# Kernel optimization log

Hardware: AMD Instinct MI355X
Metric: run time of the kernel (lower is better)

Reference implementation:

```python
import jax, jax.numpy as jnp
import numpy as np

EPS = 0.1  # residual scale from __init__


def setup_inputs() -> dict:
    key = jax.random.key(0)
    ks = jax.random.split(key, 13)
    T, B, E = 8, 4096, 16          # terms, batch(queries), predicates(edges)
    F = 1024                        # feature_dim = 2*emb_dim (emb_dim=512)
    M = 2 * F + 2                   # message_dim = 4*emb_dim + 2 = 2050
    H = 4096                        # hidden_dim

    def lin(k, fan_in, shape):
        return jax.random.normal(k, shape, jnp.float32) / np.sqrt(fan_in)

    return {
        "term_emb": jax.random.normal(ks[0], (T, B, F), jnp.float32),
        "pred_emb": jax.random.normal(ks[1], (E, B, F), jnp.float32),
        "W1": lin(ks[2], M, (M, H)),
        "b1": jnp.zeros((H,), jnp.float32),
        "W2": lin(ks[3], H, (H, F)),
        "b2": jnp.zeros((F,), jnp.float32),
        "M1": lin(ks[4], F, (F, H)),
        "mb1": jnp.zeros((H,), jnp.float32),
        "M2": lin(ks[5], H, (H, F)),
        "mb2": jnp.zeros((F,), jnp.float32),
        "head_idx": jax.random.randint(ks[6], (E,), 0, T, jnp.int32),
        "tail_idx": jax.random.randint(ks[7], (E,), 0, T, jnp.int32),
        "sign_bits": jax.random.randint(ks[8], (E,), 0, 2, jnp.int32),
    }


def reference(term_emb, pred_emb, W1, b1, W2, b2, M1, mb1, M2, mb2,
              head_idx, tail_idx, sign_bits):
    # term_emb: [T,B,F], pred_emb: [E,B,F]
    T = term_emb.shape[0]
    E, B, F = pred_emb.shape
    dt = pred_emb.dtype

    sign = (1.0 - 2.0 * sign_bits.astype(dt))[:, None, None]   # [E,1,1], +-1
    ones = jnp.ones((E, B, 1), dt)
    s_ones = sign * ones                                        # [E,B,1]

    h = term_emb[head_idx]                                      # gather [E,B,F]
    t = term_emb[tail_idx]                                      # gather [E,B,F]

    # message to head: [head_emb, pred_emb, +1, sign]
    # message to tail: [tail_emb, pred_emb, -1, sign]
    msg_h = jnp.concatenate([h, pred_emb, ones, s_ones], axis=-1)   # [E,B,M]
    msg_t = jnp.concatenate([t, pred_emb, -ones, s_ones], axis=-1)  # [E,B,M]

    msgs = jnp.concatenate([msg_h, msg_t], axis=0)              # [2E,B,M]
    seg = jnp.concatenate([head_idx, tail_idx], axis=0)         # [2E]
    agg = jax.ops.segment_sum(msgs, seg, num_segments=T)        # [T,B,M]

    # encoder MLP + eps residual
    enc = jax.nn.relu(agg @ W1 + b1) @ W2 + b2                  # [T,B,F]
    x = enc + EPS * term_emb

    # update MLP (layers == 1)
    out = jax.nn.relu(x @ M1 + mb1) @ M2 + mb2                  # [T,B,F]
    return out
```

## Files before the change

### kernel.cpp

```cpp
#include <hip/hip_runtime.h>
#include <hip/hip_bf16.h>
#include <cstdint>

typedef unsigned short u16;
typedef __attribute__((ext_vector_type(8))) u16 u16x8;
typedef __attribute__((ext_vector_type(8))) short s16x8;
typedef __attribute__((ext_vector_type(4))) float f32x4;

#define AS1(p) ((const __attribute__((address_space(1))) void*)(p))
#define AS3(p) ((__attribute__((address_space(3))) void*)(p))

__device__ __forceinline__ u16 f2bf(float f){
  union{float f; uint32_t i;} x; x.f = f;
  uint32_t r = x.i + 0x7fff + ((x.i>>16)&1);
  return (u16)(r>>16);
}

__global__ void transpose_f32_bf16(const float* __restrict__ in, u16* __restrict__ out,
                                   int K, int N){
  __shared__ u16 tile[32][33];
  const int tid = threadIdx.x;
  const int bx = blockIdx.x, by = blockIdx.y;
  const int xl = tid & 31, yl = tid >> 5;
  #pragma unroll
  for (int r = 0; r < 4; ++r){
    int y = by*32 + yl + r*8;
    tile[yl + r*8][xl] = f2bf(in[(size_t)y*N + bx*32 + xl]);
  }
  __syncthreads();
  #pragma unroll
  for (int r = 0; r < 4; ++r){
    int oy = bx*32 + yl + r*8;
    int ox = by*32 + xl;
    out[(size_t)oy*K + ox] = tile[xl][yl + r*8];
  }
}

__global__ void build_bias1(const float* __restrict__ W1, const float* __restrict__ b1,
                            const int* __restrict__ head, const int* __restrict__ tail,
                            const int* __restrict__ sign, float* __restrict__ bias1){
  int idx = blockIdx.x*256 + threadIdx.x;
  int t = idx >> 12, h = idx & 4095;
  float cH = 0.f, cS = 0.f;
  #pragma unroll
  for (int e = 0; e < 16; ++e){
    float s = 1.f - 2.f*(float)sign[e];
    if (head[e] == t){ cH += 1.f; cS += s; }
    if (tail[e] == t){ cH -= 1.f; cS += s; }
  }
  bias1[idx] = b1[h] + cH*W1[(size_t)2048*4096 + h] + cS*W1[(size_t)2049*4096 + h];
}

__global__ void build_x1(const float* __restrict__ term, const float* __restrict__ pred,
                         const int* __restrict__ head, const int* __restrict__ tail,
                         u16* __restrict__ X1, int r0){
  int idx = blockIdx.x*256 + threadIdx.x;
  int lr = idx >> 8;
  int c8 = (idx & 255) * 8;
  int grow = r0 + lr;
  int t = grow >> 12;
  int b = grow & 4095;
  float v[8];
  if (c8 < 1024){
    int deg = 0;
    #pragma unroll
    for (int e = 0; e < 16; ++e) deg += (head[e]==t) + (tail[e]==t);
    float d = (float)deg;
    const float4* p = (const float4*)(term + (size_t)grow*1024 + c8);
    float4 lo = p[0], hi = p[1];
    v[0]=d*lo.x; v[1]=d*lo.y; v[2]=d*lo.z; v[3]=d*lo.w;
    v[4]=d*hi.x; v[5]=d*hi.y; v[6]=d*hi.z; v[7]=d*hi.w;
  } else {
    int f = c8 - 1024;
    #pragma unroll
    for (int j = 0; j < 8; ++j) v[j] = 0.f;
    #pragma unroll
    for (int e = 0; e < 16; ++e){
      int w = (head[e]==t) + (tail[e]==t);
      if (w){
        const float4* p = (const float4*)(pred + ((size_t)e<<22) + ((size_t)b<<10) + f);
        float4 lo = p[0], hi = p[1];
        float fw = (float)w;
        v[0]+=fw*lo.x; v[1]+=fw*lo.y; v[2]+=fw*lo.z; v[3]+=fw*lo.w;
        v[4]+=fw*hi.x; v[5]+=fw*hi.y; v[6]+=fw*hi.z; v[7]+=fw*hi.w;
      }
    }
  }
  u16x8 o;
  #pragma unroll
  for (int j = 0; j < 8; ++j) o[j] = f2bf(v[j]);
  *(u16x8*)(X1 + (size_t)lr*2048 + c8) = o;
}

#define FENCE() asm volatile("" ::: "memory")
#define BAR()   do{ FENCE(); __builtin_amdgcn_s_barrier(); FENCE(); }while(0)
#define LGKM0() do{ asm volatile("s_waitcnt lgkmcnt(0)" ::: "memory"); \
                    __builtin_amdgcn_sched_barrier(0); }while(0)
#define SCHED0() __builtin_amdgcn_sched_barrier(0)
#define VM2()   asm volatile("s_waitcnt vmcnt(2)" ::: "memory")
#define VM4()   asm volatile("s_waitcnt vmcnt(4)" ::: "memory")

#define STAGE(isB, slot, half, kt) do{ \
    const u16* _s = (isB ? bStage : aStage) + ((half) ? halfStride : (size_t)0) + ((size_t)(kt) << 6); \
    u16* _d = &LDS[(isB ? 32768 : 0) + (slot)*16384 + (half)*8192 + tid*8]; \
    __builtin_amdgcn_global_load_lds(AS1(_s), AS3(_d), 16, 0, 0); \
    __builtin_amdgcn_global_load_lds(AS1(_s + q2s), AS3(_d + 4096), 16, 0, 0); \
  }while(0)

#define LOADA(slot, rh) do{ \
    _Pragma("unroll") \
    for (int ii = 0; ii < 4; ++ii){ \
      af[ii][0] = *(const s16x8*)&LDS[(slot)*16384 + aB + ((rh)*4+ii)*1024 + xv0]; \
      af[ii][1] = *(const s16x8*)&LDS[(slot)*16384 + aB + ((rh)*4+ii)*1024 + xv1]; \
    } }while(0)

#define LOADB01(slot) do{ \
    _Pragma("unroll") \
    for (int jj = 0; jj < 2; ++jj){ \
      bfr[jj][0] = *(const s16x8*)&LDS[32768 + (slot)*16384 + bB + jj*1024 + xv0]; \
      bfr[jj][1] = *(const s16x8*)&LDS[32768 + (slot)*16384 + bB + jj*1024 + xv1]; \
    } }while(0)

#define LOADB23(slot) do{ \
    _Pragma("unroll") \
    for (int jj = 2; jj < 4; ++jj){ \
      bfr[jj][0] = *(const s16x8*)&LDS[32768 + (slot)*16384 + bB + jj*1024 + xv0]; \
      bfr[jj][1] = *(const s16x8*)&LDS[32768 + (slot)*16384 + bB + jj*1024 + xv1]; \
    } }while(0)

#define MFMAQ(rh, ch) do{ \
    _Pragma("unroll") \
    for (int ii = 0; ii < 4; ++ii){ \
      _Pragma("unroll") \
      for (int jj = 0; jj < 2; ++jj){ \
        acc[(rh)*4+ii][(ch)*2+jj] = __builtin_amdgcn_mfma_f32_16x16x32_bf16(af[ii][0], bfr[(ch)*2+jj][0], acc[(rh)*4+ii][(ch)*2+jj], 0,0,0); \
        acc[(rh)*4+ii][(ch)*2+jj] = __builtin_amdgcn_mfma_f32_16x16x32_bf16(af[ii][1], bfr[(ch)*2+jj][1], acc[(rh)*4+ii][(ch)*2+jj], 0,0,0); \
      } } }while(0)

#define PRIO_MFMA(rh, ch) do{ \
    __builtin_amdgcn_s_setprio(1); MFMAQ(rh, ch); __builtin_amdgcn_s_setprio(0); }while(0)

template<int MODE>
__launch_bounds__(512, 2)
__global__ void gemm256(const u16* __restrict__ A, const u16* __restrict__ Bt,
                        void* __restrict__ Cv, int N, int K, int r0,
                        const float* __restrict__ bias_mat,
                        const float* __restrict__ bias_vec,
                        const float* __restrict__ resid){
  __shared__ u16 LDS[65536];
  const int tid = threadIdx.x;
  const int lane = tid & 63;
  const int wid = tid >> 6;
  const int wr = wid >> 2, wc = wid & 3;
  const int frow = lane & 15, fgrp = lane >> 4;

  int nwg = gridDim.x * gridDim.y;
  int orig = blockIdx.y * gridDim.x + blockIdx.x;
  int id = orig;
  if ((nwg & 7) == 0){ int cpx = nwg >> 3; id = (orig & 7) * cpx + (orig >> 3); }
  const int bx = id % gridDim.x, by = id / gridDim.x;
  const int row0 = by * 256, col0 = bx * 256;

  const size_t rowK = (size_t)(tid >> 3) * K;
  const int sg8 = (((tid & 7) ^ ((tid >> 3) & 7)) << 3);
  const u16* aStage = A  + (size_t)row0 * K + rowK + sg8;
  const u16* bStage = Bt + (size_t)col0 * K + rowK + sg8;
  const size_t halfStride = (size_t)128 * K;
  const size_t q2s = (size_t)64 * K;

  const int xv0 = ((fgrp)     ^ (frow & 7)) << 3;
  const int xv1 = ((4 + fgrp) ^ (frow & 7)) << 3;
  const int aB = wr * 8192 + frow * 64;
  const int bB = (wc >> 1) * 8192 + (wc & 1) * 4096 + frow * 64;

  f32x4 acc[8][4];
  #pragma unroll
  for (int i = 0; i < 8; ++i)
    #pragma unroll
    for (int j = 0; j < 4; ++j) acc[i][j] = (f32x4){0.f,0.f,0.f,0.f};
  s16x8 af[4][2], bfr[4][2];

  const int NT = K >> 6;
  const int NI = NT >> 1;

  STAGE(1,0,0,0); STAGE(1,0,1,0); STAGE(0,0,0,0); STAGE(0,0,1,0);
  STAGE(1,1,0,1); STAGE(1,1,1,1);
  VM4(); BAR(); SCHED0();

  for (int i = 0; i < NI; ++i){
    const int kt1 = 2*i + 1;
    const int kn0 = (2*i + 2 < NT) ? 2*i + 2 : NT - 2;
    const int kn1 = (2*i + 3 < NT) ? 2*i + 3 : NT - 1;
    LOADA(0,0); LOADB01(0);
    STAGE(0,1,0,kt1);
    BAR(); LGKM0();
    PRIO_MFMA(0,0);
    LOADB23(0);
    STAGE(0,1,1,kt1);
    BAR(); LGKM0();
    PRIO_MFMA(0,1);
    LOADA(0,1);
    BAR(); LGKM0();
    PRIO_MFMA(1,1);
    STAGE(1,0,0,kn0);
    VM2();
    BAR(); SCHED0();
    PRIO_MFMA(1,0);
    LOADA(1,0); LOADB01(1);
    STAGE(1,0,1,kn0);
    BAR(); LGKM0();
    PRIO_MFMA(0,0);
    LOADB23(1);
    STAGE(0,0,0,kn0);
    BAR(); LGKM0();
    PRIO_MFMA(0,1);
    LOADA(1,1);
    STAGE(0,0,1,kn0);
    BAR(); LGKM0();
    PRIO_MFMA(1,1);
    STAGE(1,1,0,kn1); STAGE(1,1,1,kn1);
    VM4();
    BAR(); SCHED0();
    PRIO_MFMA(1,0);
  }

  #pragma unroll
  for (int i2 = 0; i2 < 8; ++i2){
    #pragma unroll
    for (int j2 = 0; j2 < 4; ++j2){
      #pragma unroll
      for (int r = 0; r < 4; ++r){
        int lrow = row0 + wr*128 + i2*16 + fgrp*4 + r;
        int col  = col0 + wc*64 + j2*16 + frow;
        float v = acc[i2][j2][r];
        if (MODE == 0){
          int grow = r0 + lrow;
          v += bias_mat[(size_t)(grow >> 12)*N + col];
          v = fmaxf(v, 0.f);
          ((u16*)Cv)[(size_t)lrow*N + col] = f2bf(v);
        } else if (MODE == 1){
          int grow = r0 + lrow;
          v += bias_vec[col] + 0.1f*resid[(size_t)grow*1024 + col];
          ((u16*)Cv)[(size_t)lrow*N + col] = f2bf(v);
        } else if (MODE == 2){
          v += bias_vec[col];
          v = fmaxf(v, 0.f);
          ((u16*)Cv)[(size_t)lrow*N + col] = f2bf(v);
        } else {
          v += bias_vec[col];
          ((float*)Cv)[(size_t)lrow*N + col] = v;
        }
      }
    }
  }
}

extern "C" void kernel_launch(void* const* d_in, const int* in_sizes, int n_in,
                              void* d_out, int out_size, void* d_ws, size_t ws_size,
                              hipStream_t stream){
  const float* term = (const float*)d_in[0];
  const float* pred = (const float*)d_in[1];
  const float* W1   = (const float*)d_in[2];
  const float* b1   = (const float*)d_in[3];
  const float* W2   = (const float*)d_in[4];
  const float* b2   = (const float*)d_in[5];
  const float* M1   = (const float*)d_in[6];
  const float* mb1  = (const float*)d_in[7];
  const float* M2   = (const float*)d_in[8];
  const float* mb2  = (const float*)d_in[9];
  const int* head = (const int*)d_in[10];
  const int* tail = (const int*)d_in[11];
  const int* sign = (const int*)d_in[12];
  float* out = (float*)d_out;

  char* ws = (char*)d_ws;
  u16* W1T = (u16*)ws;  ws += (size_t)4096*2048*2;
  u16* W2T = (u16*)ws;  ws += (size_t)1024*4096*2;
  u16* M1T = (u16*)ws;  ws += (size_t)4096*1024*2;
  u16* M2T = (u16*)ws;  ws += (size_t)1024*4096*2;
  float* bias1 = (float*)ws; ws += (size_t)8*4096*4;
  size_t used = (size_t)(ws - (char*)d_ws);

  int R = 32768;
  while (R > 256 && used + (size_t)R*12288 > ws_size) R >>= 1;
  u16* bufA = (u16*)ws;
  u16* bufB = (u16*)(ws + (size_t)R*2048*2);

  transpose_f32_bf16<<<dim3(4096/32, 2048/32), 256, 0, stream>>>(W1, W1T, 2048, 4096);
  transpose_f32_bf16<<<dim3(1024/32, 4096/32), 256, 0, stream>>>(W2, W2T, 4096, 1024);
  transpose_f32_bf16<<<dim3(4096/32, 1024/32), 256, 0, stream>>>(M1, M1T, 1024, 4096);
  transpose_f32_bf16<<<dim3(1024/32, 4096/32), 256, 0, stream>>>(M2, M2T, 4096, 1024);
  build_bias1<<<dim3(8*4096/256), 256, 0, stream>>>(W1, b1, head, tail, sign, bias1);

  for (int r0 = 0; r0 < 32768; r0 += R){
    build_x1<<<dim3(R), 256, 0, stream>>>(term, pred, head, tail, bufA, r0);
    gemm256<0><<<dim3(4096/256, R/256), 512, 0, stream>>>(bufA, W1T, bufB, 4096, 2048, r0, bias1, nullptr, nullptr);
    gemm256<1><<<dim3(1024/256, R/256), 512, 0, stream>>>(bufB, W2T, bufA, 1024, 4096, r0, nullptr, b2, term);
    gemm256<2><<<dim3(4096/256, R/256), 512, 0, stream>>>(bufA, M1T, bufB, 4096, 1024, r0, nullptr, mb1, nullptr);
    gemm256<3><<<dim3(1024/256, R/256), 512, 0, stream>>>(bufB, M2T, out + (size_t)r0*1024, 1024, 4096, r0, nullptr, mb2, nullptr);
  }
}
```

Before: 1.345 ms.

## Switch GEMM inner loop from 16x16x32 to 32x32x16 bf16 MFMA tiles

Replaces the 16x16x32 MFMA fragments with 32x32x16 MFMA instructions. The LDS fragment indexing, swizzle offsets, accumulator layout (f32x16) and epilogue row/column mapping are rearranged to match. Larger MFMA tiles cut the LDS fragment reads per FLOP and the instruction count, which should ease LDS bandwidth pressure. The cost is a changed register layout and a possible rise in bank conflicts or register pressure, and the new index mapping has to be correct.

Result: slower. 1.487 ms (+10.5%).

```diff
diff --git a/kernel.cpp b/kernel.cpp
--- a/kernel.cpp
+++ b/kernel.cpp
@@ -5,7 +5,7 @@
 typedef unsigned short u16;
 typedef __attribute__((ext_vector_type(8))) u16 u16x8;
 typedef __attribute__((ext_vector_type(8))) short s16x8;
-typedef __attribute__((ext_vector_type(4))) float f32x4;
+typedef __attribute__((ext_vector_type(16))) float f32x16;
 
 #define AS1(p) ((const __attribute__((address_space(1))) void*)(p))
 #define AS3(p) ((__attribute__((address_space(3))) void*)(p))
@@ -107,38 +107,28 @@
     __builtin_amdgcn_global_load_lds(AS1(_s + q2s), AS3(_d + 4096), 16, 0, 0); \
   }while(0)
 
-#define LOADA(slot, rh) do{ \
+#define LOADA(slot, p) do{ \
     _Pragma("unroll") \
-    for (int ii = 0; ii < 4; ++ii){ \
-      af[ii][0] = *(const s16x8*)&LDS[(slot)*16384 + aB + ((rh)*4+ii)*1024 + xv0]; \
-      af[ii][1] = *(const s16x8*)&LDS[(slot)*16384 + aB + ((rh)*4+ii)*1024 + xv1]; \
+    for (int kk = 0; kk < 4; ++kk){ \
+      af[0][kk] = *(const s16x8*)&LDS[(slot)*16384 + aB + (2*(p))*2048   + xk[kk]]; \
+      af[1][kk] = *(const s16x8*)&LDS[(slot)*16384 + aB + (2*(p)+1)*2048 + xk[kk]]; \
     } }while(0)
 
-#define LOADB01(slot) do{ \
+#define LOADB(slot, cb) do{ \
     _Pragma("unroll") \
-    for (int jj = 0; jj < 2; ++jj){ \
-      bfr[jj][0] = *(const s16x8*)&LDS[32768 + (slot)*16384 + bB + jj*1024 + xv0]; \
-      bfr[jj][1] = *(const s16x8*)&LDS[32768 + (slot)*16384 + bB + jj*1024 + xv1]; \
+    for (int kk = 0; kk < 4; ++kk) \
+      bfr[cb][kk] = *(const s16x8*)&LDS[32768 + (slot)*16384 + bB + (cb)*2048 + xk[kk]]; \
+    }while(0)
+
+#define MFMAQ(p, cb) do{ \
+    _Pragma("unroll") \
+    for (int kk = 0; kk < 4; ++kk){ \
+      acc[2*(p)][cb]   = __builtin_amdgcn_mfma_f32_32x32x16_bf16(af[0][kk], bfr[cb][kk], acc[2*(p)][cb],   0,0,0); \
+      acc[2*(p)+1][cb] = __builtin_amdgcn_mfma_f32_32x32x16_bf16(af[1][kk], bfr[cb][kk], acc[2*(p)+1][cb], 0,0,0); \
     } }while(0)
 
-#define LOADB23(slot) do{ \
-    _Pragma("unroll") \
-    for (int jj = 2; jj < 4; ++jj){ \
-      bfr[jj][0] = *(const s16x8*)&LDS[32768 + (slot)*16384 + bB + jj*1024 + xv0]; \
-      bfr[jj][1] = *(const s16x8*)&LDS[32768 + (slot)*16384 + bB + jj*1024 + xv1]; \
-    } }while(0)
-
-#define MFMAQ(rh, ch) do{ \
-    _Pragma("unroll") \
-    for (int ii = 0; ii < 4; ++ii){ \
-      _Pragma("unroll") \
-      for (int jj = 0; jj < 2; ++jj){ \
-        acc[(rh)*4+ii][(ch)*2+jj] = __builtin_amdgcn_mfma_f32_16x16x32_bf16(af[ii][0], bfr[(ch)*2+jj][0], acc[(rh)*4+ii][(ch)*2+jj], 0,0,0); \
-        acc[(rh)*4+ii][(ch)*2+jj] = __builtin_amdgcn_mfma_f32_16x16x32_bf16(af[ii][1], bfr[(ch)*2+jj][1], acc[(rh)*4+ii][(ch)*2+jj], 0,0,0); \
-      } } }while(0)
-
-#define PRIO_MFMA(rh, ch) do{ \
-    __builtin_amdgcn_s_setprio(1); MFMAQ(rh, ch); __builtin_amdgcn_s_setprio(0); }while(0)
+#define PRIO_MFMA(p, cb) do{ \
+    __builtin_amdgcn_s_setprio(1); MFMAQ(p, cb); __builtin_amdgcn_s_setprio(0); }while(0)
 
 template<int MODE>
 __launch_bounds__(512, 2)
@@ -152,7 +142,7 @@
   const int lane = tid & 63;
   const int wid = tid >> 6;
   const int wr = wid >> 2, wc = wid & 3;
-  const int frow = lane & 15, fgrp = lane >> 4;
+  const int l31 = lane & 31, h = lane >> 5;
 
   int nwg = gridDim.x * gridDim.y;
   int orig = blockIdx.y * gridDim.x + blockIdx.x;
@@ -168,17 +158,20 @@
   const size_t halfStride = (size_t)128 * K;
   const size_t q2s = (size_t)64 * K;
 
-  const int xv0 = ((fgrp)     ^ (frow & 7)) << 3;
-  const int xv1 = ((4 + fgrp) ^ (frow & 7)) << 3;
-  const int aB = wr * 8192 + frow * 64;
-  const int bB = (wc >> 1) * 8192 + (wc & 1) * 4096 + frow * 64;
-
-  f32x4 acc[8][4];
-  #pragma unroll
-  for (int i = 0; i < 8; ++i)
-    #pragma unroll
-    for (int j = 0; j < 4; ++j) acc[i][j] = (f32x4){0.f,0.f,0.f,0.f};
-  s16x8 af[4][2], bfr[4][2];
+  int xk[4];
+  #pragma unroll
+  for (int kk = 0; kk < 4; ++kk) xk[kk] = ((2*kk + h) ^ (lane & 7)) << 3;
+  const int aB = wr * 8192 + l31 * 64;
+  const int bB = wc * 4096 + l31 * 64;
+
+  f32x16 acc[4][2];
+  #pragma unroll
+  for (int i = 0; i < 4; ++i)
+    #pragma unroll
+    for (int j = 0; j < 2; ++j)
+      #pragma unroll
+      for (int r = 0; r < 16; ++r) acc[i][j][r] = 0.f;
+  s16x8 af[2][4], bfr[2][4];
 
   const int NT = K >> 6;
   const int NI = NT >> 1;
@@ -191,11 +184,11 @@
     const int kt1 = 2*i + 1;
     const int kn0 = (2*i + 2 < NT) ? 2*i + 2 : NT - 2;
     const int kn1 = (2*i + 3 < NT) ? 2*i + 3 : NT - 1;
-    LOADA(0,0); LOADB01(0);
+    LOADA(0,0); LOADB(0,0);
     STAGE(0,1,0,kt1);
     BAR(); LGKM0();
     PRIO_MFMA(0,0);
-    LOADB23(0);
+    LOADB(0,1);
     STAGE(0,1,1,kt1);
     BAR(); LGKM0();
     PRIO_MFMA(0,1);
@@ -206,11 +199,11 @@
     VM2();
     BAR(); SCHED0();
     PRIO_MFMA(1,0);
-    LOADA(1,0); LOADB01(1);
+    LOADA(1,0); LOADB(1,0);
     STAGE(1,0,1,kn0);
     BAR(); LGKM0();
     PRIO_MFMA(0,0);
-    LOADB23(1);
+    LOADB(1,1);
     STAGE(0,0,0,kn0);
     BAR(); LGKM0();
     PRIO_MFMA(0,1);
@@ -225,14 +218,14 @@
   }
 
   #pragma unroll
-  for (int i2 = 0; i2 < 8; ++i2){
-    #pragma unroll
-    for (int j2 = 0; j2 < 4; ++j2){
+  for (int rb = 0; rb < 4; ++rb){
+    #pragma unroll
+    for (int cb = 0; cb < 2; ++cb){
       #pragma unroll
-      for (int r = 0; r < 4; ++r){
-        int lrow = row0 + wr*128 + i2*16 + fgrp*4 + r;
-        int col  = col0 + wc*64 + j2*16 + frow;
-        float v = acc[i2][j2][r];
+      for (int r = 0; r < 16; ++r){
+        int lrow = row0 + wr*128 + rb*32 + (r & 3) + 8*(r >> 2) + 4*h;
+        int col  = col0 + wc*64 + cb*32 + l31;
+        float v = acc[rb][cb][r];
         if (MODE == 0){
           int grow = r0 + lrow;
           v += bias_mat[(size_t)(grow >> 12)*N + col];
```
